# Kernel optimization log

Measured on AMD Instinct MI355X. Metric: run time of the kernel, lower is better.

The kernel has to match this reference:

```python
import jax, jax.numpy as jnp
import numpy as np

N_NODES = 100000
D = 256
N_EDGES = 3200000
NEG_SLOPE = 0.01  # torch F.leaky_relu default


def setup_inputs() -> dict:
    key = jax.random.key(0)
    ks = jax.random.split(key, 5)
    x = jax.random.normal(ks[0], (N_NODES, D), dtype=jnp.float32)
    edge_rows = jax.random.randint(ks[1], (N_EDGES,), 0, N_NODES, dtype=jnp.int32)
    edge_cols = jax.random.randint(ks[2], (N_EDGES,), 0, N_NODES, dtype=jnp.int32)
    edge_vals = jax.random.uniform(ks[3], (N_EDGES,), dtype=jnp.float32)
    # Linear(dim, dim) with xavier_normal_ weight, default bias init ~ U(-1/sqrt(d), 1/sqrt(d))
    std = float(np.sqrt(2.0 / (D + D)))
    W_w = jax.random.normal(ks[4], (D, D), dtype=jnp.float32) * std
    W_b = jnp.zeros((D,), dtype=jnp.float32)
    return {"x": x, "edge_rows": edge_rows, "edge_cols": edge_cols,
            "edge_vals": edge_vals, "W_w": W_w, "W_b": W_b}


def reference(x, edge_rows, edge_cols, edge_vals, W_w, W_b):
    # h = W(x)  (torch Linear: x @ W^T + b)
    h = jnp.einsum('nd,ed->ne', x, W_w) + W_b  # [n, d]
    # SpMM: out[r] = sum_e A[r, c_e] * h[c_e]  via gather + segment_sum
    msgs = edge_vals[:, None] * h[edge_cols]  # [n_edges, d]
    agg = jax.ops.segment_sum(msgs, edge_rows, num_segments=x.shape[0])  # [n, d]
    return jnp.where(agg >= 0, agg, NEG_SLOPE * agg)
```

## Files before the change

### kernel.cpp

```cpp
#include <hip/hip_runtime.h>
#include <stdint.h>

#define DIM 256
#define NEG_SLOPE 0.01f

#define NBLK 512
#define MAXK 400
#define ROWS_PER_BUCKET 256

typedef float    vfloat4 __attribute__((ext_vector_type(4)));
typedef _Float16 vhalf4  __attribute__((ext_vector_type(4)));
typedef _Float16 half8   __attribute__((ext_vector_type(8)));
typedef float    floatx4 __attribute__((ext_vector_type(4)));
typedef unsigned int vuint2 __attribute__((ext_vector_type(2)));


#define MBM 128
#define MBN 64
#define MBK 32
#define MLDP 40

__global__ __launch_bounds__(256) void gemm_xwT_kernel(
        const float* __restrict__ x, const float* __restrict__ W,
        const float* __restrict__ bias, _Float16* __restrict__ h, int M) {
    __shared__ _Float16 Ax[MBM][MLDP];
    __shared__ _Float16 Bw[MBN][MLDP];

    const int tid  = (int)threadIdx.x;
    const int row0 = blockIdx.x * MBM;
    const int col0 = blockIdx.y * MBN;
    const int wid  = tid >> 6;
    const int lane = tid & 63;
    const int wr = wid >> 1;
    const int wc = wid & 1;
    const int fr = lane & 15;
    const int fk = (lane >> 4) * 8;

    const int arow = tid >> 1;
    const int ak   = (tid & 1) * 16;
    const int wrow = tid >> 2;
    const int wk   = (tid & 3) * 8;

    floatx4 acc[4][2];
#pragma unroll
    for (int m = 0; m < 4; ++m)
#pragma unroll
        for (int n = 0; n < 2; ++n) acc[m][n] = (floatx4){0.f, 0.f, 0.f, 0.f};

    for (int kk = 0; kk < DIM; kk += MBK) {
        {
            int grow = row0 + arow;
            const float* src = &x[(size_t)grow * DIM + kk + ak];
            half8 h0, h1;
            if (grow < M) {
                vfloat4 f0 = __builtin_nontemporal_load((const vfloat4*)(src + 0));
                vfloat4 f1 = __builtin_nontemporal_load((const vfloat4*)(src + 4));
                vfloat4 f2 = __builtin_nontemporal_load((const vfloat4*)(src + 8));
                vfloat4 f3 = __builtin_nontemporal_load((const vfloat4*)(src + 12));
                h0 = (half8){(_Float16)f0.x, (_Float16)f0.y, (_Float16)f0.z, (_Float16)f0.w,
                             (_Float16)f1.x, (_Float16)f1.y, (_Float16)f1.z, (_Float16)f1.w};
                h1 = (half8){(_Float16)f2.x, (_Float16)f2.y, (_Float16)f2.z, (_Float16)f2.w,
                             (_Float16)f3.x, (_Float16)f3.y, (_Float16)f3.z, (_Float16)f3.w};
            } else {
                h0 = (half8)(_Float16)0; h1 = (half8)(_Float16)0;
            }
            *(half8*)&Ax[arow][ak]     = h0;
            *(half8*)&Ax[arow][ak + 8] = h1;
        }
        {
            const float* src = &W[(size_t)(col0 + wrow) * DIM + kk + wk];
            vfloat4 f0 = *(const vfloat4*)(src + 0);
            vfloat4 f1 = *(const vfloat4*)(src + 4);
            half8 hb = (half8){(_Float16)f0.x, (_Float16)f0.y, (_Float16)f0.z, (_Float16)f0.w,
                               (_Float16)f1.x, (_Float16)f1.y, (_Float16)f1.z, (_Float16)f1.w};
            *(half8*)&Bw[wrow][wk] = hb;
        }
        __syncthreads();

        half8 a[4], b[2];
#pragma unroll
        for (int m = 0; m < 4; ++m)
            a[m] = *(const half8*)&Ax[wr * 64 + m * 16 + fr][fk];
#pragma unroll
        for (int n = 0; n < 2; ++n)
            b[n] = *(const half8*)&Bw[wc * 32 + n * 16 + fr][fk];
#pragma unroll
        for (int m = 0; m < 4; ++m)
#pragma unroll
            for (int n = 0; n < 2; ++n)
                acc[m][n] = __builtin_amdgcn_mfma_f32_16x16x32_f16(a[m], b[n], acc[m][n], 0, 0, 0);
        __syncthreads();
    }

#pragma unroll
    for (int m = 0; m < 4; ++m) {
#pragma unroll
        for (int n = 0; n < 2; ++n) {
            int col = col0 + wc * 32 + n * 16 + fr;
            float bv = bias[col];
#pragma unroll
            for (int j = 0; j < 4; ++j) {
                int row = row0 + wr * 64 + m * 16 + (lane >> 4) * 4 + j;
                if (row < M)
                    h[(size_t)row * DIM + col] = (_Float16)(acc[m][n][j] + bv);
            }
        }
    }
}


__device__ inline int wave_incl_scan(int v) {
    const int lane = threadIdx.x & 63;
#pragma unroll
    for (int off = 1; off < 64; off <<= 1) {
        int t = __shfl_up(v, off, 64);
        if (lane >= off) v += t;
    }
    return v;
}

__global__ __launch_bounds__(256) void hist2_kernel(const int* __restrict__ rows,
        int* __restrict__ hist2, int E, int K, int chunk) {
    __shared__ int lh[MAXK];
    const int tid = (int)threadIdx.x;
    const int b = (int)blockIdx.x;
    for (int i = tid; i < K; i += 256) lh[i] = 0;
    __syncthreads();
    const int beg = b * chunk;
    const int end = min(beg + chunk, E);
    for (int i = beg + tid; i < end; i += 256)
        atomicAdd(&lh[__builtin_nontemporal_load(&rows[i]) >> 8], 1);
    __syncthreads();
    for (int i = tid; i < K; i += 256) hist2[i * NBLK + b] = lh[i];
}

__global__ __launch_bounds__(64) void scanA_kernel(int* __restrict__ hist2,
        int* __restrict__ total, int K) {
    const int k = (int)blockIdx.x;
    const int lane = (int)threadIdx.x;
    int* row = &hist2[k * NBLK];
    int v[8];
    int s = 0;
#pragma unroll
    for (int i = 0; i < 8; ++i) { v[i] = row[lane * 8 + i]; s += v[i]; }
    int incl = wave_incl_scan(s);
    int run = incl - s;
#pragma unroll
    for (int i = 0; i < 8; ++i) { row[lane * 8 + i] = run; run += v[i]; }
    if (lane == 63) total[k] = incl;
}

__global__ __launch_bounds__(64) void scanB_kernel(const int* __restrict__ total,
        int* __restrict__ bbase, int K) {
    const int lane = (int)threadIdx.x;
    int run = 0;
    for (int b = 0; b < K; b += 64) {
        int i = b + lane;
        int v = (i < K) ? total[i] : 0;
        int incl = wave_incl_scan(v);
        if (i < K) bbase[i] = run + incl - v;
        run += __shfl(incl, 63, 64);
    }
}


__global__ __launch_bounds__(256) void coarse_scatter_kernel(
        const int* __restrict__ rows, const int* __restrict__ cols,
        const float* __restrict__ vals, const int* __restrict__ hist2,
        const int* __restrict__ bbase, vuint2* __restrict__ coarse,
        int E, int K, int chunk) {
    __shared__ int cur[MAXK];
    const int tid = (int)threadIdx.x;
    const int b = (int)blockIdx.x;
    for (int i = tid; i < K; i += 256) cur[i] = bbase[i] + hist2[i * NBLK + b];
    __syncthreads();
    const int beg = b * chunk;
    const int end = min(beg + chunk, E);
    for (int i = beg + tid; i < end; i += 256) {
        int r = __builtin_nontemporal_load(&rows[i]);
        int c = __builtin_nontemporal_load(&cols[i]);
        float v = __builtin_nontemporal_load(&vals[i]);
        int pos = atomicAdd(&cur[r >> 8], 1);
        vuint2 rec;
        rec.x = ((unsigned)(r & 255) << 18) | (unsigned)c;
        rec.y = __float_as_uint(v);
        coarse[pos] = rec;
    }
}


__global__ __launch_bounds__(256) void fine_sort_kernel(
        const vuint2* __restrict__ coarse, const int* __restrict__ bbase,
        vuint2* __restrict__ sorted, int* __restrict__ offs,
        int N, int E, int K) {
    __shared__ int lh[ROWS_PER_BUCKET];
    __shared__ int wtot[4];
    const int tid = (int)threadIdx.x;
    const int lane = tid & 63, wid = tid >> 6;
    const int k = (int)blockIdx.x;
    const int row0 = k * ROWS_PER_BUCKET;
    const int beg = bbase[k];
    const int end = (k + 1 < K) ? bbase[k + 1] : E;

    lh[tid] = 0;
    __syncthreads();
    for (int j = beg + tid; j < end; j += 256)
        atomicAdd(&lh[coarse[j].x >> 18], 1);
    __syncthreads();
    int v = lh[tid];
    int incl = wave_incl_scan(v);
    if (lane == 63) wtot[wid] = incl;
    __syncthreads();
    int woff = 0;
    for (int w = 0; w < wid; ++w) woff += wtot[w];
    int excl = woff + incl - v;
    lh[tid] = beg + excl;
    int row = row0 + tid;
    if (row < N) offs[row] = beg + excl;
    __syncthreads();
    for (int j = beg + tid; j < end; j += 256) {
        vuint2 rec = __builtin_nontemporal_load(&coarse[j]);
        int pos = atomicAdd(&lh[rec.x >> 18], 1);
        sorted[pos] = rec;
    }
}


__global__ __launch_bounds__(256) void agg_kernel(
        const _Float16* __restrict__ h, const vuint2* __restrict__ sorted,
        const int* __restrict__ offs, float* __restrict__ out, int N, int E) {
    const int node = blockIdx.x * 4 + ((int)threadIdx.x >> 6);
    if (node >= N) return;
    const int lane = (int)threadIdx.x & 63;
    const int beg = offs[node];
    const int end = (node + 1 < N) ? offs[node + 1] : E;

    float4 acc0 = make_float4(0.f, 0.f, 0.f, 0.f);
    float4 acc1 = make_float4(0.f, 0.f, 0.f, 0.f);

    int j = beg;
    for (; j + 7 < end; j += 8) {
        vuint2 cv[8];
        vhalf4 hv[8];
#pragma unroll
        for (int u = 0; u < 8; ++u) cv[u] = __builtin_nontemporal_load(&sorted[j + u]);
#pragma unroll
        for (int u = 0; u < 8; ++u)
            hv[u] = *(const vhalf4*)(&h[(size_t)(cv[u].x & 0x3FFFF) * DIM + lane * 4]);
#pragma unroll
        for (int u = 0; u < 8; ++u) {
            float v = __uint_as_float(cv[u].y);
            float4* a = (u & 1) ? &acc1 : &acc0;
            a->x += v * (float)hv[u].x;
            a->y += v * (float)hv[u].y;
            a->z += v * (float)hv[u].z;
            a->w += v * (float)hv[u].w;
        }
    }
    for (; j < end; ++j) {
        vuint2 cv = __builtin_nontemporal_load(&sorted[j]);
        float v = __uint_as_float(cv.y);
        vhalf4 hv = *(const vhalf4*)(&h[(size_t)(cv.x & 0x3FFFF) * DIM + lane * 4]);
        acc0.x += v * (float)hv.x; acc0.y += v * (float)hv.y;
        acc0.z += v * (float)hv.z; acc0.w += v * (float)hv.w;
    }
    vfloat4 a;
    a.x = acc0.x + acc1.x;
    a.y = acc0.y + acc1.y;
    a.z = acc0.z + acc1.z;
    a.w = acc0.w + acc1.w;
    a.x = (a.x >= 0.f) ? a.x : NEG_SLOPE * a.x;
    a.y = (a.y >= 0.f) ? a.y : NEG_SLOPE * a.y;
    a.z = (a.z >= 0.f) ? a.z : NEG_SLOPE * a.z;
    a.w = (a.w >= 0.f) ? a.w : NEG_SLOPE * a.w;
    __builtin_nontemporal_store(a, (vfloat4*)(&out[(size_t)node * DIM + lane * 4]));
}


__global__ __launch_bounds__(256) void zero_f32_kernel(float* __restrict__ p, long long n) {
    long long i = (long long)blockIdx.x * blockDim.x + threadIdx.x;
    long long stride = (long long)gridDim.x * blockDim.x;
    for (; i < n; i += stride) p[i] = 0.0f;
}

__global__ __launch_bounds__(64) void edge_atomic_kernel(
        const int* __restrict__ rows, const int* __restrict__ cols,
        const float* __restrict__ vals, const _Float16* __restrict__ h,
        float* __restrict__ out, int E) {
    const int e = blockIdx.x;
    if (e >= E) return;
    const int lane = threadIdx.x;
    const int r = rows[e];
    const int c = cols[e];
    const float v = vals[e];
    vhalf4 hv = *(const vhalf4*)(&h[(size_t)c * DIM + lane * 4]);
    float* dst = &out[(size_t)r * DIM + lane * 4];
    atomicAdd(dst + 0, v * (float)hv.x);
    atomicAdd(dst + 1, v * (float)hv.y);
    atomicAdd(dst + 2, v * (float)hv.z);
    atomicAdd(dst + 3, v * (float)hv.w);
}

__global__ __launch_bounds__(256) void leaky_kernel(float* __restrict__ p, long long n) {
    long long i = (long long)blockIdx.x * blockDim.x + threadIdx.x;
    long long stride = (long long)gridDim.x * blockDim.x;
    for (; i < n; i += stride) {
        float v = p[i];
        p[i] = (v >= 0.f) ? v : NEG_SLOPE * v;
    }
}


extern "C" void kernel_launch(void* const* d_in, const int* in_sizes, int n_in,
                              void* d_out, int out_size, void* d_ws, size_t ws_size,
                              hipStream_t stream) {
    const float* x    = (const float*)d_in[0];
    const int*   erow = (const int*)d_in[1];
    const int*   ecol = (const int*)d_in[2];
    const float* eval_ = (const float*)d_in[3];
    const float* Ww   = (const float*)d_in[4];
    const float* Wb   = (const float*)d_in[5];
    float* out = (float*)d_out;

    const int N = in_sizes[0] / DIM;
    const int E = in_sizes[1];
    const int K = (N + ROWS_PER_BUCKET - 1) / ROWS_PER_BUCKET;
    const int chunk = (E + NBLK - 1) / NBLK;

    char* p = (char*)d_ws;
    _Float16* h = (_Float16*)p;                 p += (size_t)N * DIM * sizeof(_Float16);
    int* hist2 = (int*)p;                       p += (size_t)K * NBLK * sizeof(int);
    int* total = (int*)p;                       p += (size_t)((K + 63) & ~63) * sizeof(int);
    int* bbase = (int*)p;                       p += (size_t)((K + 63) & ~63) * sizeof(int);
    int* offs = (int*)p;                        p += (size_t)N * sizeof(int);
    uintptr_t up = ((uintptr_t)p + 15) & ~(uintptr_t)15;
    vuint2* sorted = (vuint2*)up;
    size_t need_full = (size_t)((char*)sorted - (char*)d_ws) + (size_t)E * sizeof(vuint2);
    size_t need_h = (size_t)N * DIM * sizeof(_Float16);
    bool coarse_fits = ((size_t)out_size * sizeof(float)) >= (size_t)E * sizeof(vuint2);

    dim3 ggrid((N + MBM - 1) / MBM, DIM / MBN);

    if (ws_size >= need_full && K <= MAXK && coarse_fits && N <= (1 << 18)) {
        vuint2* coarse = (vuint2*)d_out;
        hist2_kernel<<<NBLK, 256, 0, stream>>>(erow, hist2, E, K, chunk);
        scanA_kernel<<<K, 64, 0, stream>>>(hist2, total, K);
        scanB_kernel<<<1, 64, 0, stream>>>(total, bbase, K);
        coarse_scatter_kernel<<<NBLK, 256, 0, stream>>>(erow, ecol, eval_, hist2,
                                                        bbase, coarse, E, K, chunk);
        fine_sort_kernel<<<K, 256, 0, stream>>>(coarse, bbase, sorted, offs, N, E, K);
        gemm_xwT_kernel<<<ggrid, 256, 0, stream>>>(x, Ww, Wb, h, N);
        agg_kernel<<<(N + 3) / 4, 256, 0, stream>>>(h, sorted, offs, out, N, E);
    } else if (ws_size >= need_h) {
        gemm_xwT_kernel<<<ggrid, 256, 0, stream>>>(x, Ww, Wb, h, N);
        zero_f32_kernel<<<2048, 256, 0, stream>>>(out, (long long)N * DIM);
        edge_atomic_kernel<<<E, 64, 0, stream>>>(erow, ecol, eval_, h, out, E);
        leaky_kernel<<<2048, 256, 0, stream>>>(out, (long long)N * DIM);
    }
}
```

Before: 498.2 us.

## Fuse sort pipeline into cooperative kernel and widen GEMM tile to full output width

The five sorting kernels (histogram, two scans, coarse scatter, fine sort) are merged into one cooperative kernel that uses grid-wide syncs between phases, with the separate launches kept as a fallback if the cooperative launch fails. This removes inter-kernel launch gaps and drain bubbles. The GEMM is retiled so each block computes 128 rows by all 256 columns, so each x row is loaded once instead of four times, at the cost of more accumulator registers (32 floatx4 per thread). scanA is also changed to use 256 threads per block.

```diff
diff --git a/kernel.cpp b/kernel.cpp
--- a/kernel.cpp
+++ b/kernel.cpp
@@ -1,5 +1,8 @@
 #include <hip/hip_runtime.h>
+#include <hip/hip_cooperative_groups.h>
 #include <stdint.h>
+
+namespace cg = cooperative_groups;
 
 #define DIM 256
 #define NEG_SLOPE 0.01f
@@ -15,92 +18,72 @@
 typedef unsigned int vuint2 __attribute__((ext_vector_type(2)));
 
 
-#define MBM 128
-#define MBN 64
-#define MBK 32
-#define MLDP 40
+#define G2M 128
+#define G2LD 36
 
 __global__ __launch_bounds__(256) void gemm_xwT_kernel(
         const float* __restrict__ x, const float* __restrict__ W,
         const float* __restrict__ bias, _Float16* __restrict__ h, int M) {
-    __shared__ _Float16 Ax[MBM][MLDP];
-    __shared__ _Float16 Bw[MBN][MLDP];
+    __shared__ _Float16 Ax[G2M][G2LD];
+    __shared__ _Float16 Bw[DIM][G2LD];
 
     const int tid  = (int)threadIdx.x;
-    const int row0 = blockIdx.x * MBM;
-    const int col0 = blockIdx.y * MBN;
-    const int wid  = tid >> 6;
+    const int row0 = blockIdx.x * G2M;
+    const int w    = tid >> 6;
     const int lane = tid & 63;
-    const int wr = wid >> 1;
-    const int wc = wid & 1;
     const int fr = lane & 15;
-    const int fk = (lane >> 4) * 8;
-
-    const int arow = tid >> 1;
-    const int ak   = (tid & 1) * 16;
-    const int wrow = tid >> 2;
-    const int wk   = (tid & 3) * 8;
-
-    floatx4 acc[4][2];
-#pragma unroll
-    for (int m = 0; m < 4; ++m)
-#pragma unroll
-        for (int n = 0; n < 2; ++n) acc[m][n] = (floatx4){0.f, 0.f, 0.f, 0.f};
-
-    for (int kk = 0; kk < DIM; kk += MBK) {
-        {
-            int grow = row0 + arow;
-            const float* src = &x[(size_t)grow * DIM + kk + ak];
-            half8 h0, h1;
-            if (grow < M) {
-                vfloat4 f0 = __builtin_nontemporal_load((const vfloat4*)(src + 0));
-                vfloat4 f1 = __builtin_nontemporal_load((const vfloat4*)(src + 4));
-                vfloat4 f2 = __builtin_nontemporal_load((const vfloat4*)(src + 8));
-                vfloat4 f3 = __builtin_nontemporal_load((const vfloat4*)(src + 12));
-                h0 = (half8){(_Float16)f0.x, (_Float16)f0.y, (_Float16)f0.z, (_Float16)f0.w,
-                             (_Float16)f1.x, (_Float16)f1.y, (_Float16)f1.z, (_Float16)f1.w};
-                h1 = (half8){(_Float16)f2.x, (_Float16)f2.y, (_Float16)f2.z, (_Float16)f2.w,
-                             (_Float16)f3.x, (_Float16)f3.y, (_Float16)f3.z, (_Float16)f3.w};
-            } else {
-                h0 = (half8)(_Float16)0; h1 = (half8)(_Float16)0;
-            }
-            *(half8*)&Ax[arow][ak]     = h0;
-            *(half8*)&Ax[arow][ak + 8] = h1;
-        }
-        {
-            const float* src = &W[(size_t)(col0 + wrow) * DIM + kk + wk];
-            vfloat4 f0 = *(const vfloat4*)(src + 0);
-            vfloat4 f1 = *(const vfloat4*)(src + 4);
-            half8 hb = (half8){(_Float16)f0.x, (_Float16)f0.y, (_Float16)f0.z, (_Float16)f0.w,
-                               (_Float16)f1.x, (_Float16)f1.y, (_Float16)f1.z, (_Float16)f1.w};
-            *(half8*)&Bw[wrow][wk] = hb;
-        }
-        __syncthreads();
-
-        half8 a[4], b[2];
-#pragma unroll
-        for (int m = 0; m < 4; ++m)
-            a[m] = *(const half8*)&Ax[wr * 64 + m * 16 + fr][fk];
-#pragma unroll
-        for (int n = 0; n < 2; ++n)
-            b[n] = *(const half8*)&Bw[wc * 32 + n * 16 + fr][fk];
-#pragma unroll
-        for (int m = 0; m < 4; ++m)
-#pragma unroll
-            for (int n = 0; n < 2; ++n)
-                acc[m][n] = __builtin_amdgcn_mfma_f32_16x16x32_f16(a[m], b[n], acc[m][n], 0, 0, 0);
-        __syncthreads();
-    }
-
-#pragma unroll
-    for (int m = 0; m < 4; ++m) {
-#pragma unroll
-        for (int n = 0; n < 2; ++n) {
-            int col = col0 + wc * 32 + n * 16 + fr;
-            float bv = bias[col];
+    const int fq = lane >> 4;
+    const int fk = fq * 8;
+
+    const int srow = tid >> 3;
+    const int sk4  = (tid & 7) * 4;
+
+    floatx4 acc[2][16];
+#pragma unroll
+    for (int m = 0; m < 2; ++m)
+#pragma unroll
+        for (int n = 0; n < 16; ++n) acc[m][n] = (floatx4){0.f, 0.f, 0.f, 0.f};
+
+    for (int kk = 0; kk < DIM; kk += 32) {
+#pragma unroll
+        for (int i = 0; i < 4; ++i) {
+            int r = i * 32 + srow;
+            int grow = row0 + r;
+            vfloat4 f = {0.f, 0.f, 0.f, 0.f};
+            if (grow < M)
+                f = __builtin_nontemporal_load((const vfloat4*)(&x[(size_t)grow * DIM + kk + sk4]));
+            vhalf4 hv = {(_Float16)f.x, (_Float16)f.y, (_Float16)f.z, (_Float16)f.w};
+            *(vhalf4*)&Ax[r][sk4] = hv;
+        }
+#pragma unroll
+        for (int i = 0; i < 8; ++i) {
+            int c = i * 32 + srow;
+            vfloat4 f = *(const vfloat4*)(&W[(size_t)c * DIM + kk + sk4]);
+            vhalf4 hv = {(_Float16)f.x, (_Float16)f.y, (_Float16)f.z, (_Float16)f.w};
+            *(vhalf4*)&Bw[c][sk4] = hv;
+        }
+        __syncthreads();
+
+        half8 a0 = *(const half8*)&Ax[w * 32 + fr][fk];
+        half8 a1 = *(const half8*)&Ax[w * 32 + 16 + fr][fk];
+#pragma unroll
+        for (int n = 0; n < 16; ++n) {
+            half8 bf = *(const half8*)&Bw[n * 16 + fr][fk];
+            acc[0][n] = __builtin_amdgcn_mfma_f32_16x16x32_f16(a0, bf, acc[0][n], 0, 0, 0);
+            acc[1][n] = __builtin_amdgcn_mfma_f32_16x16x32_f16(a1, bf, acc[1][n], 0, 0, 0);
+        }
+        __syncthreads();
+    }
+
+#pragma unroll
+    for (int n = 0; n < 16; ++n) {
+        int col = n * 16 + fr;
+        float bv = bias[col];
+#pragma unroll
+        for (int m = 0; m < 2; ++m) {
 #pragma unroll
             for (int j = 0; j < 4; ++j) {
-                int row = row0 + wr * 64 + m * 16 + (lane >> 4) * 4 + j;
+                int row = row0 + w * 32 + m * 16 + fq * 4 + j;
                 if (row < M)
                     h[(size_t)row * DIM + col] = (_Float16)(acc[m][n][j] + bv);
             }
@@ -118,6 +101,100 @@
     }
     return v;
 }
+
+
+__global__ __launch_bounds__(256) void sort_coop_kernel(
+        const int* __restrict__ rows, const int* __restrict__ cols,
+        const float* __restrict__ vals, int* __restrict__ hist2,
+        int* __restrict__ total, int* __restrict__ bbase,
+        vuint2* __restrict__ coarse, vuint2* __restrict__ sorted,
+        int* __restrict__ offs, int E, int K, int N, int chunk) {
+    cg::grid_group grid = cg::this_grid();
+    __shared__ int lh[MAXK];
+    __shared__ int wtot[4];
+    const int tid = (int)threadIdx.x;
+    const int b = (int)blockIdx.x;
+    const int lane = tid & 63, wid = tid >> 6;
+    const int beg = b * chunk;
+    const int end = min(beg + chunk, E);
+
+    for (int i = tid; i < K; i += 256) lh[i] = 0;
+    __syncthreads();
+    for (int i = beg + tid; i < end; i += 256)
+        atomicAdd(&lh[__builtin_nontemporal_load(&rows[i]) >> 8], 1);
+    __syncthreads();
+    for (int i = tid; i < K; i += 256) hist2[i * NBLK + b] = lh[i];
+    grid.sync();
+
+    if (b < K) {
+        int* row = &hist2[b * NBLK];
+        int v0 = row[tid * 2], v1 = row[tid * 2 + 1];
+        int s = v0 + v1;
+        int incl = wave_incl_scan(s);
+        if (lane == 63) wtot[wid] = incl;
+        __syncthreads();
+        int woff = 0;
+        for (int ww = 0; ww < wid; ++ww) woff += wtot[ww];
+        int excl = woff + incl - s;
+        row[tid * 2] = excl;
+        row[tid * 2 + 1] = excl + v0;
+        if (tid == 255) total[b] = woff + incl;
+    }
+    grid.sync();
+
+    if (b == 0 && wid == 0) {
+        int run = 0;
+        for (int base = 0; base < K; base += 64) {
+            int i = base + lane;
+            int v = (i < K) ? total[i] : 0;
+            int incl = wave_incl_scan(v);
+            if (i < K) bbase[i] = run + incl - v;
+            run += __shfl(incl, 63, 64);
+        }
+    }
+    grid.sync();
+
+    for (int i = tid; i < K; i += 256) lh[i] = bbase[i] + hist2[i * NBLK + b];
+    __syncthreads();
+    for (int i = beg + tid; i < end; i += 256) {
+        int r = __builtin_nontemporal_load(&rows[i]);
+        int c = __builtin_nontemporal_load(&cols[i]);
+        float v = __builtin_nontemporal_load(&vals[i]);
+        int pos = atomicAdd(&lh[r >> 8], 1);
+        vuint2 rec;
+        rec.x = ((unsigned)(r & 255) << 18) | (unsigned)c;
+        rec.y = __float_as_uint(v);
+        coarse[pos] = rec;
+    }
+    grid.sync();
+
+    if (b < K) {
+        const int row0 = b * ROWS_PER_BUCKET;
+        const int fbeg = bbase[b];
+        const int fend = (b + 1 < K) ? bbase[b + 1] : E;
+        if (tid < ROWS_PER_BUCKET) lh[tid] = 0;
+        __syncthreads();
+        for (int j = fbeg + tid; j < fend; j += 256)
+            atomicAdd(&lh[coarse[j].x >> 18], 1);
+        __syncthreads();
+        int v = lh[tid];
+        int incl = wave_incl_scan(v);
+        if (lane == 63) wtot[wid] = incl;
+        __syncthreads();
+        int woff = 0;
+        for (int ww = 0; ww < wid; ++ww) woff += wtot[ww];
+        int excl = woff + incl - v;
+        lh[tid] = fbeg + excl;
+        if (row0 + tid < N) offs[row0 + tid] = fbeg + excl;
+        __syncthreads();
+        for (int j = fbeg + tid; j < fend; j += 256) {
+            vuint2 rec = __builtin_nontemporal_load(&coarse[j]);
+            int pos = atomicAdd(&lh[rec.x >> 18], 1);
+            sorted[pos] = rec;
+        }
+    }
+}
+
 
 __global__ __launch_bounds__(256) void hist2_kernel(const int* __restrict__ rows,
         int* __restrict__ hist2, int E, int K, int chunk) {
@@ -134,20 +211,24 @@
     for (int i = tid; i < K; i += 256) hist2[i * NBLK + b] = lh[i];
 }
 
-__global__ __launch_bounds__(64) void scanA_kernel(int* __restrict__ hist2,
+__global__ __launch_bounds__(256) void scanA_kernel(int* __restrict__ hist2,
         int* __restrict__ total, int K) {
+    __shared__ int wtot[4];
+    const int tid = (int)threadIdx.x;
+    const int lane = tid & 63, wid = tid >> 6;
     const int k = (int)blockIdx.x;
-    const int lane = (int)threadIdx.x;
     int* row = &hist2[k * NBLK];
-    int v[8];
-    int s = 0;
-#pragma unroll
-    for (int i = 0; i < 8; ++i) { v[i] = row[lane * 8 + i]; s += v[i]; }
+    int v0 = row[tid * 2], v1 = row[tid * 2 + 1];
+    int s = v0 + v1;
     int incl = wave_incl_scan(s);
-    int run = incl - s;
-#pragma unroll
-    for (int i = 0; i < 8; ++i) { row[lane * 8 + i] = run; run += v[i]; }
-    if (lane == 63) total[k] = incl;
+    if (lane == 63) wtot[wid] = incl;
+    __syncthreads();
+    int woff = 0;
+    for (int ww = 0; ww < wid; ++ww) woff += wtot[ww];
+    int excl = woff + incl - s;
+    row[tid * 2] = excl;
+    row[tid * 2 + 1] = excl + v0;
+    if (tid == 255) total[k] = woff + incl;
 }
 
 __global__ __launch_bounds__(64) void scanB_kernel(const int* __restrict__ total,
@@ -162,7 +243,6 @@
         run += __shfl(incl, 63, 64);
     }
 }
-
 
 __global__ __launch_bounds__(256) void coarse_scatter_kernel(
         const int* __restrict__ rows, const int* __restrict__ cols,
@@ -187,7 +267,6 @@
         coarse[pos] = rec;
     }
 }
-
 
 __global__ __launch_bounds__(256) void fine_sort_kernel(
         const vuint2* __restrict__ coarse, const int* __restrict__ bbase,
@@ -201,7 +280,6 @@
     const int row0 = k * ROWS_PER_BUCKET;
     const int beg = bbase[k];
     const int end = (k + 1 < K) ? bbase[k + 1] : E;
-
     lh[tid] = 0;
     __syncthreads();
     for (int j = beg + tid; j < end; j += 256)
@@ -212,11 +290,10 @@
     if (lane == 63) wtot[wid] = incl;
     __syncthreads();
     int woff = 0;
-    for (int w = 0; w < wid; ++w) woff += wtot[w];
+    for (int ww = 0; ww < wid; ++ww) woff += wtot[ww];
     int excl = woff + incl - v;
     lh[tid] = beg + excl;
-    int row = row0 + tid;
-    if (row < N) offs[row] = beg + excl;
+    if (row0 + tid < N) offs[row0 + tid] = beg + excl;
     __syncthreads();
     for (int j = beg + tid; j < end; j += 256) {
         vuint2 rec = __builtin_nontemporal_load(&coarse[j]);
@@ -339,16 +416,28 @@
     size_t need_h = (size_t)N * DIM * sizeof(_Float16);
     bool coarse_fits = ((size_t)out_size * sizeof(float)) >= (size_t)E * sizeof(vuint2);
 
-    dim3 ggrid((N + MBM - 1) / MBM, DIM / MBN);
+    dim3 ggrid((N + G2M - 1) / G2M);
 
     if (ws_size >= need_full && K <= MAXK && coarse_fits && N <= (1 << 18)) {
         vuint2* coarse = (vuint2*)d_out;
-        hist2_kernel<<<NBLK, 256, 0, stream>>>(erow, hist2, E, K, chunk);
-        scanA_kernel<<<K, 64, 0, stream>>>(hist2, total, K);
-        scanB_kernel<<<1, 64, 0, stream>>>(total, bbase, K);
-        coarse_scatter_kernel<<<NBLK, 256, 0, stream>>>(erow, ecol, eval_, hist2,
-                                                        bbase, coarse, E, K, chunk);
-        fine_sort_kernel<<<K, 256, 0, stream>>>(coarse, bbase, sorted, offs, N, E, K);
+        {
+            const int* a_rows = erow; const int* a_cols = ecol; const float* a_vals = eval_;
+            int* a_h2 = hist2; int* a_tot = total; int* a_bb = bbase;
+            vuint2* a_co = coarse; vuint2* a_so = sorted; int* a_off = offs;
+            int a_E = E, a_K = K, a_N = N, a_ch = chunk;
+            void* args[] = {&a_rows, &a_cols, &a_vals, &a_h2, &a_tot, &a_bb,
+                            &a_co, &a_so, &a_off, &a_E, &a_K, &a_N, &a_ch};
+            hipError_t ce = hipLaunchCooperativeKernel((void*)sort_coop_kernel,
+                                dim3(NBLK), dim3(256), args, 0, stream);
+            if (ce != hipSuccess) {
+                hist2_kernel<<<NBLK, 256, 0, stream>>>(erow, hist2, E, K, chunk);
+                scanA_kernel<<<K, 256, 0, stream>>>(hist2, total, K);
+                scanB_kernel<<<1, 64, 0, stream>>>(total, bbase, K);
+                coarse_scatter_kernel<<<NBLK, 256, 0, stream>>>(erow, ecol, eval_,
+                        hist2, bbase, coarse, E, K, chunk);
+                fine_sort_kernel<<<K, 256, 0, stream>>>(coarse, bbase, sorted, offs, N, E, K);
+            }
+        }
         gemm_xwT_kernel<<<ggrid, 256, 0, stream>>>(x, Ww, Wb, h, N);
         agg_kernel<<<(N + 3) / 4, 256, 0, stream>>>(h, sorted, offs, out, N, E);
     } else if (ws_size >= need_h) {
```

Result: slower. 795.6 us (+59.7%).
